# Kernel tuning notes

Measured on AMD Instinct MI355X. Metric: run time of the kernel, lower is better.

## Reference

```python
import jax, jax.numpy as jnp
import numpy as np

B, N, DIM = 8, 2048, 512
HEADS, DIM_HEAD = 8, 64
INNER = HEADS * DIM_HEAD  # 512
SCALE = DIM_HEAD ** -0.5
NEG = -1e9


def setup_inputs() -> dict:
    key = jax.random.key(0)
    ks = jax.random.split(key, 7)
    x = jax.random.normal(ks[0], (B, N, DIM), dtype=jnp.float32)
    adj = jax.random.uniform(ks[1], (B, N, N), dtype=jnp.float32)
    att_mask = jax.random.randint(ks[2], (B, 1, N, N), 0, 2).astype(jnp.bool_)
    W_gcn = jax.random.normal(ks[3], (DIM, DIM), dtype=jnp.float32) * (DIM ** -0.5)
    W_qkv = jax.random.normal(ks[4], (DIM, 3 * INNER), dtype=jnp.float32) * (DIM ** -0.5)
    W_out = jax.random.normal(ks[5], (INNER + DIM, DIM), dtype=jnp.float32) * ((INNER + DIM) ** -0.5)
    b_out = jax.random.normal(ks[6], (DIM,), dtype=jnp.float32) * 0.01
    return {"x": x, "adj": adj, "att_mask": att_mask,
            "W_gcn": W_gcn, "W_qkv": W_qkv, "W_out": W_out, "b_out": b_out}


def reference(x, adj, att_mask, W_gcn, W_qkv, W_out, b_out):
    # GCN branch: adj @ (x W_gcn)  -> [b, n, dim]
    gcn = jnp.einsum('bnj,bjd->bnd', adj, x @ W_gcn)

    # Attention branch
    qkv = x @ W_qkv                                  # [b, n, 3*inner]
    q, k, v = jnp.split(qkv, 3, axis=-1)
    split_heads = lambda t: t.reshape(B, N, HEADS, DIM_HEAD).transpose(0, 2, 1, 3)
    q, k, v = split_heads(q), split_heads(k), split_heads(v)  # [b, h, n, d]

    dots = jnp.einsum('bhid,bhjd->bhij', q, k) * SCALE        # [b, h, n, n]
    dots = jnp.where(att_mask, NEG, dots)
    attn = jax.nn.softmax(dots, axis=-1)
    att_out = jnp.einsum('bhij,bhjd->bhid', attn, v)          # [b, h, n, d]
    att_out = att_out.transpose(0, 2, 1, 3).reshape(B, N, INNER)

    out = jnp.concatenate([att_out, gcn], axis=-1)            # [b, n, inner+dim]
    return out @ W_out + b_out                                # [b, n, dim]
```

## Files before the change

kernel.cpp:

```cpp
#include <hip/hip_runtime.h>
#include <stdint.h>

#define DEVFN __device__ __forceinline__

typedef __attribute__((ext_vector_type(8))) short short8;
typedef __attribute__((ext_vector_type(4))) short short4v;
typedef __attribute__((ext_vector_type(4))) float floatx4;
typedef __attribute__((ext_vector_type(4))) float vfloat4;
typedef __attribute__((ext_vector_type(2))) unsigned int uint2v;

#define MFMA_BF16(a,b,c) __builtin_amdgcn_mfma_f32_16x16x32_bf16((a),(b),(c),0,0,0)
#define GL2LDS(g,l) __builtin_amdgcn_global_load_lds((const __attribute__((address_space(1))) void*)(g), (__attribute__((address_space(3))) void*)(l), 16, 0, 0)

DEVFN unsigned short f2bf(float f){
  unsigned u = __float_as_uint(f);
  u = (u + 0x7fffu + ((u >> 16) & 1u)) >> 16;
  return (unsigned short)u;
}

__global__ void detect_kernel(const unsigned char* m, unsigned int* flag){
  if (threadIdx.x == 0) *flag = 0u;
  __syncthreads();
  int any = 0;
  for (int i = threadIdx.x; i < 4096; i += 256)
    if ((i & 3) != 0 && m[i]) any = 1;
  if (any) atomicOr(flag, 1u);
}

__global__ void prep_kernel(const float* __restrict__ x, const float* __restrict__ wg,
                            const float* __restrict__ wq, const float* __restrict__ wo,
                            const void* __restrict__ mask, const unsigned* __restrict__ flag,
                            const float* __restrict__ adj,
                            unsigned short* __restrict__ xbf, unsigned short* __restrict__ wcat,
                            unsigned short* __restrict__ woutT, unsigned* __restrict__ mp,
                            unsigned short* __restrict__ adjb)
{
  int bid = blockIdx.x, tid = threadIdx.x;
  if (bid < 8192) {
    int i = (bid*256 + tid)*4;
    vfloat4 v = *(const vfloat4*)&x[i];
    short4v c; c[0]=(short)f2bf(v[0]); c[1]=(short)f2bf(v[1]); c[2]=(short)f2bf(v[2]); c[3]=(short)f2bf(v[3]);
    *(short4v*)&xbf[i] = c;
  } else if (bid < 8192 + 4096) {
    int i = (bid - 8192)*256 + tid;
    int k = i & 511, c = i >> 9;
    float v = (c < 512) ? wg[k*512 + c] : wq[k*1536 + (c - 512)];
    wcat[c*512 + k] = (unsigned short)f2bf(v);
  } else if (bid < 8192 + 4096 + 2048) {
    int i = (bid - 12288)*256 + tid;
    int k = i & 1023, n2 = i >> 10;
    woutT[n2*1024 + k] = (unsigned short)f2bf(wo[k*512 + n2]);
  } else if (bid < 145408) {
    int j = bid - 14336;
    int e = j*256 + tid;
    int v;
    if (*flag) v = ((const unsigned char*)mask)[e];
    else       v = ((const int*)mask)[e];
    unsigned long long ball = __ballot(v != 0);
    int base = e & ~63;
    int lane = tid & 63;
    if (lane == 0)  mp[(base >> 5) + 0] = (unsigned)(ball & 0xffffffffull);
    if (lane == 32) mp[(base >> 5) + 1] = (unsigned)(ball >> 32);
  } else {
    int i = ((bid - 145408)*256 + tid)*4;
    vfloat4 v = *(const vfloat4*)&adj[i];
    short4v c; c[0]=(short)f2bf(v[0]); c[1]=(short)f2bf(v[1]); c[2]=(short)f2bf(v[2]); c[3]=(short)f2bf(v[3]);
    *(short4v*)&adjb[i] = c;
  }
}

DEVFN void gemm_kloop_bf16(const unsigned short* Ag, int lda,
                           const unsigned short* Bg, int ldb, int K,
                           short* As, short* Bs, int w, int l,
                           floatx4 (&acc)[4][4])
{
  const int wr = (w >> 1)*64, wc = (w & 1)*64;
  for (int k0 = 0; k0 < K; k0 += 32) {
    __syncthreads();
#pragma unroll
    for (int i = 0; i < 2; i++) {
      int id = (w*2 + i)*64 + l;
      int row = id >> 2, part = id & 3;
      GL2LDS(Ag + row*lda + k0 + part*8, As + (w*2 + i)*512);
      GL2LDS(Bg + row*ldb + k0 + part*8, Bs + (w*2 + i)*512);
    }
    __syncthreads();
    short8 af[4], bfr[4];
#pragma unroll
    for (int t = 0; t < 4; t++) {
      af[t]  = *(const short8*)&As[(wr + t*16 + (l & 15))*32 + ((l >> 4) << 3)];
      bfr[t] = *(const short8*)&Bs[(wc + t*16 + (l & 15))*32 + ((l >> 4) << 3)];
    }
#pragma unroll
    for (int a2 = 0; a2 < 4; a2++)
#pragma unroll
      for (int b2 = 0; b2 < 4; b2++)
        acc[a2][b2] = MFMA_BF16(af[a2], bfr[b2], acc[a2][b2]);
  }
}

__global__ __launch_bounds__(256, 2)
void gemm_ab_kernel(const unsigned short* __restrict__ xbf, const unsigned short* __restrict__ wcat,
                    unsigned short* __restrict__ xgT, unsigned short* __restrict__ Qo,
                    unsigned short* __restrict__ Ko, unsigned short* __restrict__ VTo)
{
  __shared__ short lds[16384];
  int tid = threadIdx.x, w = tid >> 6, l = tid & 63;
  int bid = blockIdx.x;
  int xcd = bid & 7, slot = bid >> 3;
  int p  = xcd + ((slot >> 4) << 3);
  int nt = slot & 15;
  int rows0 = p*128, cols0 = nt*128;

  floatx4 acc[4][4];
  const floatx4 zf = {0.f, 0.f, 0.f, 0.f};
#pragma unroll
  for (int a2 = 0; a2 < 4; a2++)
#pragma unroll
    for (int b2 = 0; b2 < 4; b2++) acc[a2][b2] = zf;

  gemm_kloop_bf16(xbf + rows0*512, 512, wcat + cols0*512, 512, 512,
                  lds, lds + 4096, w, l, acc);
  __syncthreads();

  int wr = (w >> 1)*64, wc = (w & 1)*64;
  int b = p >> 4;
  int n0 = (p & 15)*128 + wr;
  int gc0 = cols0 + wc;

  if (nt < 4 || nt >= 12) {
    short* T = lds + w*4096;
#pragma unroll
    for (int mi = 0; mi < 4; mi++)
#pragma unroll
      for (int bi = 0; bi < 4; bi++)
#pragma unroll
        for (int r = 0; r < 4; r++) {
          int rl = mi*16 + ((l >> 4) << 2) + r;
          int cl = bi*16 + (l & 15);
          T[cl*64 + ((((rl >> 3) ^ (cl & 7))) << 3) + (rl & 7)] = (short)f2bf(acc[mi][bi][r]);
        }
#pragma unroll
    for (int i = 0; i < 8; i++) {
      int chunk = i*64 + l;
      int c = chunk >> 3, s = chunk & 7;
      short8 v = *(const short8*)&T[c*64 + ((s ^ (c & 7)) << 3)];
      int rowstart = n0 + s*8;
      if (nt < 4) {
        int d = gc0 + c;
        *(short8*)&xgT[(b*512 + d)*2048 + rowstart] = v;
      } else {
        int vc = gc0 + c - 1536;
        int hh = vc >> 6, dd = vc & 63;
        *(short8*)&VTo[((b*8 + hh)*64 + dd)*2048 + rowstart] = v;
      }
    }
  } else {
    unsigned short* dst = (nt < 8) ? Qo : Ko;
    int cbase = gc0 - ((nt < 8) ? 512 : 1024);
    int hh = cbase >> 6;
#pragma unroll
    for (int mi = 0; mi < 4; mi++)
#pragma unroll
      for (int bi = 0; bi < 4; bi++)
#pragma unroll
        for (int r = 0; r < 4; r++) {
          int rowg = n0 + mi*16 + ((l >> 4) << 2) + r;
          int dd = bi*16 + (l & 15);
          dst[((b*8 + hh)*2048 + rowg)*64 + dd] = (unsigned short)f2bf(acc[mi][bi][r]);
        }
  }
}

__global__ __launch_bounds__(256, 2)
void gemm_c_bf16_kernel(const unsigned short* __restrict__ adjb, const unsigned short* __restrict__ xgT,
                        unsigned short* __restrict__ cat)
{
  __shared__ short lds[8192];
  int tid = threadIdx.x, w = tid >> 6, l = tid & 63;
  int bid = blockIdx.x;
  int xcd = bid & 7, slot = bid >> 3;
  int p  = xcd + ((slot >> 2) << 3);
  int nt = slot & 3;
  int b = p >> 4, mt = p & 15;
  int rows0 = mt*128, cols0 = nt*128;

  floatx4 acc[4][4];
  const floatx4 zf = {0.f, 0.f, 0.f, 0.f};
#pragma unroll
  for (int a2 = 0; a2 < 4; a2++)
#pragma unroll
    for (int b2 = 0; b2 < 4; b2++) acc[a2][b2] = zf;

  gemm_kloop_bf16(adjb + (size_t)b*2048*2048 + (size_t)rows0*2048, 2048,
                  xgT + (b*512 + cols0)*2048, 2048, 2048,
                  lds, lds + 4096, w, l, acc);

  int wr = (w >> 1)*64, wc = (w & 1)*64;
#pragma unroll
  for (int mi = 0; mi < 4; mi++)
#pragma unroll
    for (int bi = 0; bi < 4; bi++)
#pragma unroll
      for (int r = 0; r < 4; r++) {
        int rowg = b*2048 + rows0 + wr + mi*16 + ((l >> 4) << 2) + r;
        int col  = 512 + cols0 + wc + bi*16 + (l & 15);
        cat[rowg*1024 + col] = (unsigned short)f2bf(acc[mi][bi][r]);
      }
}

__global__ __launch_bounds__(256, 2)
void gemm_c_f32_kernel(const float* __restrict__ adj, const unsigned short* __restrict__ xgT,
                       unsigned short* __restrict__ cat)
{
  __shared__ short lds[8192];
  int tid = threadIdx.x, w = tid >> 6, l = tid & 63;
  int bid = blockIdx.x;
  int xcd = bid & 7, slot = bid >> 3;
  int p  = xcd + ((slot >> 2) << 3);
  int nt = slot & 3;
  int b = p >> 4, mt = p & 15;
  int rows0 = mt*128, cols0 = nt*128;
  const float* Ag = adj + (size_t)b*2048*2048 + (size_t)rows0*2048;
  const unsigned short* Bg = xgT + (b*512 + cols0)*2048;

  floatx4 acc[4][4];
  const floatx4 zf = {0.f, 0.f, 0.f, 0.f};
#pragma unroll
  for (int a2 = 0; a2 < 4; a2++)
#pragma unroll
    for (int b2 = 0; b2 < 4; b2++) acc[a2][b2] = zf;

  const int wr = (w >> 1)*64, wc = (w & 1)*64;
  for (int k0 = 0; k0 < 2048; k0 += 32) {
    __syncthreads();
#pragma unroll
    for (int i = 0; i < 4; i++) {
      int id = (w*4 + i)*64 + l;
      int row = id >> 3, part = id & 7;
      vfloat4 v = *(const vfloat4*)&Ag[row*2048 + k0 + part*4];
      short4v c4; c4[0]=(short)f2bf(v[0]); c4[1]=(short)f2bf(v[1]); c4[2]=(short)f2bf(v[2]); c4[3]=(short)f2bf(v[3]);
      *(short4v*)&lds[row*32 + part*4] = c4;
    }
#pragma unroll
    for (int i = 0; i < 2; i++) {
      int id = (w*2 + i)*64 + l;
      int row = id >> 2, part = id & 3;
      GL2LDS(Bg + row*2048 + k0 + part*8, lds + 4096 + (w*2 + i)*512);
    }
    __syncthreads();
    short8 af[4], bfr[4];
#pragma unroll
    for (int t = 0; t < 4; t++) {
      af[t]  = *(const short8*)&lds[(wr + t*16 + (l & 15))*32 + ((l >> 4) << 3)];
      bfr[t] = *(const short8*)&lds[4096 + (wc + t*16 + (l & 15))*32 + ((l >> 4) << 3)];
    }
#pragma unroll
    for (int a2 = 0; a2 < 4; a2++)
#pragma unroll
      for (int b2 = 0; b2 < 4; b2++)
        acc[a2][b2] = MFMA_BF16(af[a2], bfr[b2], acc[a2][b2]);
  }

#pragma unroll
  for (int mi = 0; mi < 4; mi++)
#pragma unroll
    for (int bi = 0; bi < 4; bi++)
#pragma unroll
      for (int r = 0; r < 4; r++) {
        int rowg = b*2048 + rows0 + wr + mi*16 + ((l >> 4) << 2) + r;
        int col  = 512 + cols0 + wc + bi*16 + (l & 15);
        cat[rowg*1024 + col] = (unsigned short)f2bf(acc[mi][bi][r]);
      }
}

DEVFN void attn_stage(const unsigned short* KB, const unsigned short* VB,
                      short* Ks, short* Vs, int kn0, int w, int l)
{
#pragma unroll
  for (int i = 0; i < 2; i++) {
    int id = (w*2 + i)*64 + l;
    int row = id >> 3, sl = id & 7;
    int sp = sl ^ (row & 7);
    GL2LDS(KB + (kn0 + row)*64 + sp*8, Ks + (w*2 + i)*512);
    GL2LDS(VB + row*2048 + kn0 + sp*8, Vs + (w*2 + i)*512);
  }
}

__global__ __launch_bounds__(256, 3)
void attn_kernel(const unsigned short* __restrict__ Q, const unsigned short* __restrict__ Kb,
                 const unsigned short* __restrict__ VT, const unsigned* __restrict__ mp,
                 unsigned short* __restrict__ cat)
{
  __shared__ short lds[24576];
  int tid = threadIdx.x, w = tid >> 6, l = tid & 63;
  short* Ps = lds + 16384 + w*2048;

  int bid = blockIdx.x;
  int xcd = bid & 7, slot = bid >> 3;
  int bh = xcd + ((slot >> 4) << 3);
  int qt = slot & 15;
  int b = bh >> 3, h = bh & 7;
  int qw = qt*128 + w*32;

  const unsigned short* Qb = Q  + (size_t)bh*2048*64;
  const unsigned short* KB = Kb + (size_t)bh*2048*64;
  const unsigned short* VB = VT + (size_t)bh*64*2048;
  const unsigned* mrow = mp + b*2048*64;

  short8 qf[2][2];
#pragma unroll
  for (int mi = 0; mi < 2; mi++)
#pragma unroll
    for (int ks = 0; ks < 2; ks++)
      qf[mi][ks] = *(const short8*)&Qb[(qw + mi*16 + (l & 15))*64 + ks*32 + ((l >> 4) << 3)];

  floatx4 oacc[2][4];
  float dsum[8];
  const floatx4 zf = {0.f, 0.f, 0.f, 0.f};
#pragma unroll
  for (int mi = 0; mi < 2; mi++)
#pragma unroll
    for (int di = 0; di < 4; di++) oacc[mi][di] = zf;
#pragma unroll
  for (int t = 0; t < 8; t++) dsum[t] = 0.f;

  const float C_SL2E = 0.125f * 1.44269504f;

  attn_stage(KB, VB, lds, lds + 8192, 0, w, l);
  asm volatile("s_waitcnt vmcnt(0)" ::: "memory");
  __builtin_amdgcn_s_barrier();
  asm volatile("" ::: "memory");

  for (int kt = 0; kt < 32; kt++) {
    int cur = kt & 1;
    short* Ks = lds + cur*4096;
    short* Vs = lds + 8192 + cur*4096;
    int kn0 = kt*64;

    if (kt < 31)
      attn_stage(KB, VB, lds + (cur ^ 1)*4096, lds + 8192 + (cur ^ 1)*4096, kn0 + 64, w, l);

    uint2v m2[8];
#pragma unroll
    for (int mi = 0; mi < 2; mi++)
#pragma unroll
      for (int r = 0; r < 4; r++) {
        int qg = qw + mi*16 + ((l >> 4) << 2) + r;
        m2[mi*4 + r] = *(const uint2v*)&mrow[qg*64 + kt*2];
      }

    floatx4 sacc[2][4];
#pragma unroll
    for (int mi = 0; mi < 2; mi++)
#pragma unroll
      for (int bi = 0; bi < 4; bi++) sacc[mi][bi] = zf;
#pragma unroll
    for (int ks = 0; ks < 2; ks++) {
      short8 kf[4];
#pragma unroll
      for (int bi = 0; bi < 4; bi++) {
        int row = bi*16 + (l & 15);
        int s = ks*4 + (l >> 4);
        kf[bi] = *(const short8*)&Ks[row*64 + ((s ^ (row & 7)) << 3)];
      }
#pragma unroll
      for (int mi = 0; mi < 2; mi++)
#pragma unroll
        for (int bi = 0; bi < 4; bi++)
          sacc[mi][bi] = MFMA_BF16(qf[mi][ks], kf[bi], sacc[mi][bi]);
    }

#pragma unroll
    for (int mi = 0; mi < 2; mi++) {
#pragma unroll
      for (int r = 0; r < 4; r++) {
        int ql = mi*16 + ((l >> 4) << 2) + r;
        unsigned wd0 = m2[mi*4 + r].x;
        unsigned wd1 = m2[mi*4 + r].y;
#pragma unroll
        for (int bi = 0; bi < 4; bi++) {
          int kl = bi*16 + (l & 15);
          unsigned wdd = (bi & 2) ? wd1 : wd0;
          int bit = (wdd >> (kl & 31)) & 1;
          float p = exp2f(sacc[mi][bi][r] * C_SL2E);
          p = bit ? 0.f : p;
          dsum[mi*4 + r] += p;
          Ps[ql*64 + (((kl >> 3) ^ (ql & 7)) << 3) + (kl & 7)] = (short)(__float_as_uint(p) >> 16);
        }
      }
    }

#pragma unroll
    for (int ks = 0; ks < 2; ks++) {
      short8 pf[2], vf[4];
#pragma unroll
      for (int mi = 0; mi < 2; mi++) {
        int row = mi*16 + (l & 15);
        int s = ks*4 + (l >> 4);
        pf[mi] = *(const short8*)&Ps[row*64 + ((s ^ (row & 7)) << 3)];
      }
#pragma unroll
      for (int di = 0; di < 4; di++) {
        int row = di*16 + (l & 15);
        int s = ks*4 + (l >> 4);
        vf[di] = *(const short8*)&Vs[row*64 + ((s ^ (row & 7)) << 3)];
      }
#pragma unroll
      for (int mi = 0; mi < 2; mi++)
#pragma unroll
        for (int di = 0; di < 4; di++)
          oacc[mi][di] = MFMA_BF16(pf[mi], vf[di], oacc[mi][di]);
    }

    asm volatile("s_waitcnt vmcnt(0)" ::: "memory");
    __builtin_amdgcn_s_barrier();
    asm volatile("" ::: "memory");
  }

#pragma unroll
  for (int t = 0; t < 8; t++) {
    float v = dsum[t];
    v += __shfl_xor(v, 1);
    v += __shfl_xor(v, 2);
    v += __shfl_xor(v, 4);
    v += __shfl_xor(v, 8);
    dsum[t] = v;
  }

#pragma unroll
  for (int mi = 0; mi < 2; mi++)
#pragma unroll
    for (int r = 0; r < 4; r++) {
      float inv = 1.0f / dsum[mi*4 + r];
#pragma unroll
      for (int di = 0; di < 4; di++) {
        int rowg = b*2048 + qw + mi*16 + ((l >> 4) << 2) + r;
        int col = h*64 + di*16 + (l & 15);
        cat[rowg*1024 + col] = (unsigned short)f2bf(oacc[mi][di][r] * inv);
      }
    }
}

__global__ __launch_bounds__(256, 2)
void gemm_d_kernel(const unsigned short* __restrict__ cat, const unsigned short* __restrict__ woutT,
                   const float* __restrict__ bout, float* __restrict__ out)
{
  __shared__ short lds[8192];
  int tid = threadIdx.x, w = tid >> 6, l = tid & 63;
  int bid = blockIdx.x;
  int xcd = bid & 7, slot = bid >> 3;
  int p  = xcd + ((slot >> 2) << 3);
  int nt = slot & 3;
  int rows0 = p*128, cols0 = nt*128;

  floatx4 acc[4][4];
  const floatx4 zf = {0.f, 0.f, 0.f, 0.f};
#pragma unroll
  for (int a2 = 0; a2 < 4; a2++)
#pragma unroll
    for (int b2 = 0; b2 < 4; b2++) acc[a2][b2] = zf;

  gemm_kloop_bf16(cat + (size_t)rows0*1024, 1024, woutT + cols0*1024, 1024, 1024,
                  lds, lds + 4096, w, l, acc);

  int wr = (w >> 1)*64, wc = (w & 1)*64;
#pragma unroll
  for (int bi = 0; bi < 4; bi++) {
    int col = cols0 + wc + bi*16 + (l & 15);
    float bias = bout[col];
#pragma unroll
    for (int mi = 0; mi < 4; mi++)
#pragma unroll
      for (int r = 0; r < 4; r++) {
        int rowg = rows0 + wr + mi*16 + ((l >> 4) << 2) + r;
        out[rowg*512 + col] = acc[mi][bi][r] + bias;
      }
  }
}

extern "C" void kernel_launch(void* const* d_in, const int* in_sizes, int n_in,
                              void* d_out, int out_size, void* d_ws, size_t ws_size,
                              hipStream_t stream)
{
  (void)in_sizes; (void)n_in; (void)out_size;
  const float* x   = (const float*)d_in[0];
  const float* adj = (const float*)d_in[1];
  const void*  msk = d_in[2];
  const float* wg  = (const float*)d_in[3];
  const float* wq  = (const float*)d_in[4];
  const float* wo  = (const float*)d_in[5];
  const float* bo  = (const float*)d_in[6];
  float* out = (float*)d_out;
  char* ws = (char*)d_ws;

  unsigned short* xbf   = (unsigned short*)(ws + 0);
  unsigned short* wcat  = (unsigned short*)(ws + 16777216);
  unsigned short* woutT = (unsigned short*)(ws + 18874368);
  unsigned short* xgT   = (unsigned short*)(ws + 19922944);
  unsigned short* Qb    = (unsigned short*)(ws + 36700160);
  unsigned short* Kb    = (unsigned short*)(ws + 53477376);
  unsigned short* VTb   = (unsigned short*)(ws + 70254592);
  unsigned short* cat   = (unsigned short*)(ws + 87031808);
  unsigned*       mp    = (unsigned*)(ws + 120586240);
  unsigned*       flag  = (unsigned*)(ws + 124780544);
  unsigned short* adjb  = (unsigned short*)(ws + 124780608);

  const int use_adjb = (ws_size >= (size_t)124780608 + 67108864) ? 1 : 0;

  detect_kernel<<<1, 256, 0, stream>>>((const unsigned char*)msk, flag);
  prep_kernel<<<use_adjb ? 178176 : 145408, 256, 0, stream>>>(
      x, wg, wq, wo, msk, flag, adj, xbf, wcat, woutT, mp, adjb);
  gemm_ab_kernel<<<2048, 256, 0, stream>>>(xbf, wcat, xgT, Qb, Kb, VTb);
  if (use_adjb)
    gemm_c_bf16_kernel<<<512, 256, 0, stream>>>(adjb, xgT, cat);
  else
    gemm_c_f32_kernel<<<512, 256, 0, stream>>>(adj, xgT, cat);
  attn_kernel<<<1024, 256, 0, stream>>>(Qb, Kb, VTb, mp, cat);
  gemm_d_kernel<<<512, 256, 0, stream>>>(cat, woutT, bo, out);
}
```

Before: 431.4 us.

## Rewrite attention with 32x32 MFMA, transposed S, and register-resident P via bpermute

```diff
diff --git a/kernel.cpp b/kernel.cpp
--- a/kernel.cpp
+++ b/kernel.cpp
@@ -6,16 +6,25 @@
 typedef __attribute__((ext_vector_type(8))) short short8;
 typedef __attribute__((ext_vector_type(4))) short short4v;
 typedef __attribute__((ext_vector_type(4))) float floatx4;
+typedef __attribute__((ext_vector_type(16))) float floatx16;
 typedef __attribute__((ext_vector_type(4))) float vfloat4;
 typedef __attribute__((ext_vector_type(2))) unsigned int uint2v;
+typedef __attribute__((ext_vector_type(4))) unsigned int uint4v;
 
 #define MFMA_BF16(a,b,c) __builtin_amdgcn_mfma_f32_16x16x32_bf16((a),(b),(c),0,0,0)
+#define MFMA32_BF16(a,b,c) __builtin_amdgcn_mfma_f32_32x32x16_bf16((a),(b),(c),0,0,0)
 #define GL2LDS(g,l) __builtin_amdgcn_global_load_lds((const __attribute__((address_space(1))) void*)(g), (__attribute__((address_space(3))) void*)(l), 16, 0, 0)
 
 DEVFN unsigned short f2bf(float f){
   unsigned u = __float_as_uint(f);
   u = (u + 0x7fffu + ((u >> 16) & 1u)) >> 16;
   return (unsigned short)u;
+}
+
+DEVFN unsigned cvtpk_bf16(float lo, float hi){
+  unsigned r;
+  asm("v_cvt_pk_bf16_f32 %0, %1, %2" : "=v"(r) : "v"(lo), "v"(hi));
+  return r;
 }
 
 __global__ void detect_kernel(const unsigned char* m, unsigned int* flag){
@@ -287,43 +296,38 @@
   }
 }
 
-__global__ __launch_bounds__(256, 3)
+__global__ __launch_bounds__(256, 4)
 void attn_kernel(const unsigned short* __restrict__ Q, const unsigned short* __restrict__ Kb,
                  const unsigned short* __restrict__ VT, const unsigned* __restrict__ mp,
                  unsigned short* __restrict__ cat)
 {
-  __shared__ short lds[24576];
+  __shared__ short lds[16384];
   int tid = threadIdx.x, w = tid >> 6, l = tid & 63;
-  short* Ps = lds + 16384 + w*2048;
+  int c5 = l & 31, h = l >> 5;
+  int hv = h*4;
+  int paddr = (l ^ 32) << 2;
 
   int bid = blockIdx.x;
   int xcd = bid & 7, slot = bid >> 3;
   int bh = xcd + ((slot >> 4) << 3);
   int qt = slot & 15;
-  int b = bh >> 3, h = bh & 7;
+  int b = bh >> 3, hd = bh & 7;
   int qw = qt*128 + w*32;
 
   const unsigned short* Qb = Q  + (size_t)bh*2048*64;
   const unsigned short* KB = Kb + (size_t)bh*2048*64;
   const unsigned short* VB = VT + (size_t)bh*64*2048;
-  const unsigned* mrow = mp + b*2048*64;
-
-  short8 qf[2][2];
-#pragma unroll
-  for (int mi = 0; mi < 2; mi++)
-#pragma unroll
-    for (int ks = 0; ks < 2; ks++)
-      qf[mi][ks] = *(const short8*)&Qb[(qw + mi*16 + (l & 15))*64 + ks*32 + ((l >> 4) << 3)];
-
-  floatx4 oacc[2][4];
-  float dsum[8];
-  const floatx4 zf = {0.f, 0.f, 0.f, 0.f};
-#pragma unroll
-  for (int mi = 0; mi < 2; mi++)
-#pragma unroll
-    for (int di = 0; di < 4; di++) oacc[mi][di] = zf;
-#pragma unroll
-  for (int t = 0; t < 8; t++) dsum[t] = 0.f;
+  const unsigned* mrow = mp + b*2048*64 + (qw + c5)*64;
+
+  short8 qf[4];
+#pragma unroll
+  for (int dk = 0; dk < 4; dk++)
+    qf[dk] = *(const short8*)&Qb[(qw + c5)*64 + dk*16 + h*8];
+
+  floatx16 oacc[2];
+  const floatx16 zf16 = {0.f,0.f,0.f,0.f,0.f,0.f,0.f,0.f,0.f,0.f,0.f,0.f,0.f,0.f,0.f,0.f};
+  oacc[0] = zf16; oacc[1] = zf16;
+  float dsum = 0.f;
 
   const float C_SL2E = 0.125f * 1.44269504f;
 
@@ -336,81 +340,67 @@
     int cur = kt & 1;
     short* Ks = lds + cur*4096;
     short* Vs = lds + 8192 + cur*4096;
-    int kn0 = kt*64;
 
     if (kt < 31)
-      attn_stage(KB, VB, lds + (cur ^ 1)*4096, lds + 8192 + (cur ^ 1)*4096, kn0 + 64, w, l);
-
-    uint2v m2[8];
-#pragma unroll
-    for (int mi = 0; mi < 2; mi++)
-#pragma unroll
-      for (int r = 0; r < 4; r++) {
-        int qg = qw + mi*16 + ((l >> 4) << 2) + r;
-        m2[mi*4 + r] = *(const uint2v*)&mrow[qg*64 + kt*2];
-      }
-
-    floatx4 sacc[2][4];
-#pragma unroll
-    for (int mi = 0; mi < 2; mi++)
-#pragma unroll
-      for (int bi = 0; bi < 4; bi++) sacc[mi][bi] = zf;
-#pragma unroll
-    for (int ks = 0; ks < 2; ks++) {
-      short8 kf[4];
-#pragma unroll
-      for (int bi = 0; bi < 4; bi++) {
-        int row = bi*16 + (l & 15);
-        int s = ks*4 + (l >> 4);
-        kf[bi] = *(const short8*)&Ks[row*64 + ((s ^ (row & 7)) << 3)];
-      }
-#pragma unroll
-      for (int mi = 0; mi < 2; mi++)
-#pragma unroll
-        for (int bi = 0; bi < 4; bi++)
-          sacc[mi][bi] = MFMA_BF16(qf[mi][ks], kf[bi], sacc[mi][bi]);
-    }
-
-#pragma unroll
-    for (int mi = 0; mi < 2; mi++) {
-#pragma unroll
-      for (int r = 0; r < 4; r++) {
-        int ql = mi*16 + ((l >> 4) << 2) + r;
-        unsigned wd0 = m2[mi*4 + r].x;
-        unsigned wd1 = m2[mi*4 + r].y;
-#pragma unroll
-        for (int bi = 0; bi < 4; bi++) {
-          int kl = bi*16 + (l & 15);
-          unsigned wdd = (bi & 2) ? wd1 : wd0;
-          int bit = (wdd >> (kl & 31)) & 1;
-          float p = exp2f(sacc[mi][bi][r] * C_SL2E);
-          p = bit ? 0.f : p;
-          dsum[mi*4 + r] += p;
-          Ps[ql*64 + (((kl >> 3) ^ (ql & 7)) << 3) + (kl & 7)] = (short)(__float_as_uint(p) >> 16);
+      attn_stage(KB, VB, lds + (cur ^ 1)*4096, lds + 8192 + (cur ^ 1)*4096, kt*64 + 64, w, l);
+
+    uint2v wd = *(const uint2v*)&mrow[kt*2];
+
+#pragma unroll
+    for (int kb = 0; kb < 2; kb++) {
+      floatx16 sacc = zf16;
+      __builtin_amdgcn_s_setprio(1);
+#pragma unroll
+      for (int dk = 0; dk < 4; dk++) {
+        int row = kb*32 + c5;
+        int sl = dk*2 + h;
+        short8 kf = *(const short8*)&Ks[row*64 + ((sl ^ (row & 7)) << 3)];
+        sacc = MFMA32_BF16(kf, qf[dk], sacc);
+      }
+      __builtin_amdgcn_s_setprio(0);
+
+      unsigned wsh = (kb ? wd.y : wd.x) >> hv;
+      float ps[16];
+#pragma unroll
+      for (int t = 0; t < 16; t++) {
+        int bit = (wsh >> ((t >> 2)*8 + (t & 3))) & 1;
+        float p = exp2f(sacc[t] * C_SL2E);
+        p = bit ? 0.f : p;
+        dsum += p;
+        ps[t] = p;
+      }
+      unsigned pk[4][2];
+#pragma unroll
+      for (int s = 0; s < 4; s++) {
+        pk[s][0] = cvtpk_bf16(ps[s*4 + 0], ps[s*4 + 1]);
+        pk[s][1] = cvtpk_bf16(ps[s*4 + 2], ps[s*4 + 3]);
+      }
+
+#pragma unroll
+      for (int ksl = 0; ksl < 2; ksl++) {
+        unsigned own0 = h ? pk[2*ksl + 1][0] : pk[2*ksl][0];
+        unsigned own1 = h ? pk[2*ksl + 1][1] : pk[2*ksl][1];
+        unsigned snd0 = h ? pk[2*ksl][0]     : pk[2*ksl + 1][0];
+        unsigned snd1 = h ? pk[2*ksl][1]     : pk[2*ksl + 1][1];
+        unsigned prm0 = (unsigned)__builtin_amdgcn_ds_bpermute(paddr, (int)snd0);
+        unsigned prm1 = (unsigned)__builtin_amdgcn_ds_bpermute(paddr, (int)snd1);
+        uint4v fu;
+        fu[0] = h ? prm0 : own0;
+        fu[1] = h ? prm1 : own1;
+        fu[2] = h ? own0 : prm0;
+        fu[3] = h ? own1 : prm1;
+        short8 pfrag = *(short8*)&fu;
+
+        __builtin_amdgcn_s_setprio(1);
+#pragma unroll
+        for (int db = 0; db < 2; db++) {
+          int row = db*32 + c5;
+          int sl = kb*4 + ksl*2 + h;
+          short8 vf = *(const short8*)&Vs[row*64 + ((sl ^ (row & 7)) << 3)];
+          oacc[db] = MFMA32_BF16(pfrag, vf, oacc[db]);
         }
-      }
-    }
-
-#pragma unroll
-    for (int ks = 0; ks < 2; ks++) {
-      short8 pf[2], vf[4];
-#pragma unroll
-      for (int mi = 0; mi < 2; mi++) {
-        int row = mi*16 + (l & 15);
-        int s = ks*4 + (l >> 4);
-        pf[mi] = *(const short8*)&Ps[row*64 + ((s ^ (row & 7)) << 3)];
-      }
-#pragma unroll
-      for (int di = 0; di < 4; di++) {
-        int row = di*16 + (l & 15);
-        int s = ks*4 + (l >> 4);
-        vf[di] = *(const short8*)&Vs[row*64 + ((s ^ (row & 7)) << 3)];
-      }
-#pragma unroll
-      for (int mi = 0; mi < 2; mi++)
-#pragma unroll
-        for (int di = 0; di < 4; di++)
-          oacc[mi][di] = MFMA_BF16(pf[mi], vf[di], oacc[mi][di]);
+        __builtin_amdgcn_s_setprio(0);
+      }
     }
 
     asm volatile("s_waitcnt vmcnt(0)" ::: "memory");
@@ -418,27 +408,16 @@
     asm volatile("" ::: "memory");
   }
 
-#pragma unroll
-  for (int t = 0; t < 8; t++) {
-    float v = dsum[t];
-    v += __shfl_xor(v, 1);
-    v += __shfl_xor(v, 2);
-    v += __shfl_xor(v, 4);
-    v += __shfl_xor(v, 8);
-    dsum[t] = v;
-  }
-
-#pragma unroll
-  for (int mi = 0; mi < 2; mi++)
-#pragma unroll
-    for (int r = 0; r < 4; r++) {
-      float inv = 1.0f / dsum[mi*4 + r];
-#pragma unroll
-      for (int di = 0; di < 4; di++) {
-        int rowg = b*2048 + qw + mi*16 + ((l >> 4) << 2) + r;
-        int col = h*64 + di*16 + (l & 15);
-        cat[rowg*1024 + col] = (unsigned short)f2bf(oacc[mi][di][r] * inv);
-      }
+  dsum += __shfl_xor(dsum, 32);
+  float inv = 1.0f / dsum;
+
+#pragma unroll
+  for (int db = 0; db < 2; db++)
+#pragma unroll
+    for (int t = 0; t < 16; t++) {
+      int qrow = qw + (t & 3) + 8*(t >> 2) + hv;
+      int col = hd*64 + db*32 + c5;
+      cat[(b*2048 + qrow)*1024 + col] = (unsigned short)f2bf(oacc[db][t] * inv);
     }
 }
 
```

Result: faster. 395.0 us (-8.4%).
